# Kernel optimization log

Hardware: AMD Instinct MI355X
Metric: run time of the kernel (lower is better)

## Reference

```python
import jax, jax.numpy as jnp
import numpy as np


def setup_inputs() -> dict:
    key = jax.random.key(0)
    k1, k2, k3 = jax.random.split(key, 3)
    B, S, E = 2, 2048, 2048
    H, O, A = 16, 1024, 128  # heads, codebook options, head_size (E = H*A)
    x = jax.random.normal(k1, (B, S, E), dtype=jnp.float32)
    vq_head_weights = jax.random.normal(k2, (H, O, A), dtype=jnp.float32) * 0.02
    vq_codebooks = jax.random.normal(k3, (H, O, A), dtype=jnp.float32) * 0.02
    temperature = jnp.ones((1,), dtype=jnp.float32)
    return {"x": x, "vq_head_weights": vq_head_weights, "vq_codebooks": vq_codebooks, "temperature": temperature}


def reference(x, vq_head_weights, vq_codebooks, temperature):
    # Training-mode, frozen, use_temperature=True path (straight-through VQ):
    # probs = one_hot(argmax(logits)) + softmax(logits/T) - stop_grad(softmax(logits/T))
    B, S, E = x.shape
    H, O, A = vq_head_weights.shape
    x_prepped = x.reshape(B, S, H, A)
    logits = jnp.einsum('bsha,hoa->bsho', x_prepped, vq_head_weights)
    probs = jax.nn.softmax(logits / temperature[0], axis=-1)
    argmax = jnp.argmax(logits, axis=-1)  # [B,S,H]
    hard_probs = jax.nn.one_hot(argmax, O, dtype=logits.dtype)
    probs = hard_probs + probs - jax.lax.stop_gradient(probs)
    out = jnp.einsum('bsho,hoa->bsha', probs, vq_codebooks)
    return out.reshape(B, S, E)
```

## Files before the change

kernel.cpp:

```cpp
#include <hip/hip_runtime.h>

typedef _Float16 half8 __attribute__((ext_vector_type(8)));
typedef float    f32x16 __attribute__((ext_vector_type(16)));

constexpr int kH = 16;
constexpr int kO = 1024;
constexpr int kA = 128;
constexpr int kBS = 4096;
constexpr int MTILE = 64;
constexpr int NITER = 16;

typedef const __attribute__((address_space(1))) uint32_t* gas_ptr;
typedef __attribute__((address_space(3))) uint32_t* las_ptr;

__global__ void split_w(const float* __restrict__ w, ushort* __restrict__ wp) {
    const int lane = threadIdx.x & 63;
    const int gw   = blockIdx.x * 4 + (threadIdx.x >> 6);
    const int ks   = lane >> 3;
    const int half = (lane >> 2) & 1;
    const int j    = (2 * lane) & 7;
#pragma unroll
    for (int q = 0; q < 4; ++q) {
        int r = gw * 4 + q;
        int h = r >> 10, o = r & 1023, t = o >> 5, o31 = o & 31;
        float2 v = *(const float2*)(w + r * kA + lane * 2);
        _Float16 h0 = (_Float16)v.x, h1 = (_Float16)v.y;
        _Float16 l0 = (_Float16)(v.x - (float)h0), l1 = (_Float16)(v.y - (float)h1);
        ushort2 hv = { __builtin_bit_cast(ushort, h0), __builtin_bit_cast(ushort, h1) };
        ushort2 lv = { __builtin_bit_cast(ushort, l0), __builtin_bit_cast(ushort, l1) };
        ushort* d = wp + (h * 32 + t) * 8192 + ks * 512 + (half * 32 + o31) * 8 + j;
        *(ushort2*)d = hv;
        *(ushort2*)(d + 4096) = lv;
    }
}

__launch_bounds__(256, 2)
__global__ void vq_argmax_gather(const float* __restrict__ x,
                                 const ushort* __restrict__ wp,
                                 const float* __restrict__ cb,
                                 float* __restrict__ out) {
    __shared__ ushort wtile[2][2][8192];
    __shared__ float red_max[2][MTILE];
    __shared__ int   red_idx[2][MTILE];

    const int tid   = threadIdx.x;
    const int lane  = tid & 63;
    const int wv    = tid >> 6;
    const int nhalf = wv >> 1;
    const int mtile = wv & 1;
    const int bid   = blockIdx.x;
    const int h  = ((bid & 7) << 1) | ((bid >> 3) & 1);
    const int p0 = (bid >> 4) * MTILE;

    const int l31  = lane & 31;
    const int half = lane >> 5;

    const ushort* wh_base = wp + h * 32 * 8192;

    auto stage = [&](int it, int buf) {
#pragma unroll
        for (int q = 0; q < 8; ++q) {
            int c   = wv * 8 + q;
            int nh  = c >> 4, rem = c & 15;
            const ushort* g = wh_base + (nh * 16 + it) * 8192 + rem * 512 + lane * 8;
            ushort* l = &wtile[buf][nh][rem * 512];
            __builtin_amdgcn_global_load_lds((gas_ptr)(const void*)g,
                                             (las_ptr)(void*)l, 16, 0, 0);
        }
    };

    stage(0, 0);

    const int mrow = p0 + mtile * 32 + l31;
    const float* xbase = x + (mrow * kH + h) * kA + half * 8;
    half8 xh[8], xl[8];
#pragma unroll
    for (int ks = 0; ks < 8; ++ks) {
        float4 v0 = *(const float4*)(xbase + ks * 16);
        float4 v1 = *(const float4*)(xbase + ks * 16 + 4);
        float va[8] = { v0.x, v0.y, v0.z, v0.w, v1.x, v1.y, v1.z, v1.w };
        half8 hi, lo;
#pragma unroll
        for (int j = 0; j < 8; ++j) {
            _Float16 hj = (_Float16)va[j];
            hi[j] = hj;
            lo[j] = (_Float16)(va[j] - (float)hj);
        }
        xh[ks] = hi; xl[ks] = lo;
    }

    float best = -1e30f;
    int   bidx = 0;
    const int nwb = nhalf * (kO / 2);

    __syncthreads();

    for (int it = 0; it < NITER; ++it) {
        const int cur = it & 1;
        if (it + 1 < NITER) stage(it + 1, cur ^ 1);

        const ushort* lbase = &wtile[cur][nhalf][lane * 8];
        half8 wh[8], wl[8];
#pragma unroll
        for (int ks = 0; ks < 8; ++ks) {
            wh[ks] = *(const half8*)(lbase + ks * 512);
            wl[ks] = *(const half8*)(lbase + 4096 + ks * 512);
        }
        f32x16 acc = {};
#pragma unroll
        for (int ks = 0; ks < 8; ++ks)
            acc = __builtin_amdgcn_mfma_f32_32x32x16_f16(wh[ks], xh[ks], acc, 0, 0, 0);
#pragma unroll
        for (int ks = 0; ks < 8; ++ks)
            acc = __builtin_amdgcn_mfma_f32_32x32x16_f16(wh[ks], xl[ks], acc, 0, 0, 0);
#pragma unroll
        for (int ks = 0; ks < 8; ++ks)
            acc = __builtin_amdgcn_mfma_f32_32x32x16_f16(wl[ks], xh[ks], acc, 0, 0, 0);

        float lv = acc[0];
        int   lr = 0;
#pragma unroll
        for (int r = 1; r < 16; ++r) {
            if (acc[r] > lv) { lv = acc[r]; lr = r; }
        }
        int li = nwb + it * 32 + 4 * half + (lr & 3) + 8 * (lr >> 2);
        if (lv > best) { best = lv; bidx = li; }

        __syncthreads();
    }

    {
        float om = __shfl_xor(best, 32, 64);
        int   oi = __shfl_xor(bidx, 32, 64);
        if (om > best || (om == best && oi < bidx)) { best = om; bidx = oi; }
    }
    if (half == 0) {
        red_max[nhalf][mtile * 32 + l31] = best;
        red_idx[nhalf][mtile * 32 + l31] = bidx;
    }
    __syncthreads();

    for (int i = tid; i < MTILE * 32; i += 256) {
        int row = i >> 5, ch = i & 31;
        float m0 = red_max[0][row], m1 = red_max[1][row];
        int o = (m1 > m0) ? red_idx[1][row] : red_idx[0][row];
        float4 v = *(const float4*)(cb + (h * kO + o) * kA + ch * 4);
        *(float4*)(out + ((p0 + row) * kH + h) * kA + ch * 4) = v;
    }
}

extern "C" void kernel_launch(void* const* d_in, const int* in_sizes, int n_in,
                              void* d_out, int out_size, void* d_ws, size_t ws_size,
                              hipStream_t stream) {
    const float* x  = (const float*)d_in[0];
    const float* w  = (const float*)d_in[1];
    const float* cb = (const float*)d_in[2];
    float* out = (float*)d_out;

    ushort* wpacked = (ushort*)d_ws;

    split_w<<<dim3(1024), dim3(256), 0, stream>>>(w, wpacked);
    vq_argmax_gather<<<dim3((kBS / MTILE) * kH), dim3(256), 0, stream>>>(x, wpacked, cb, out);
}
```

Measured before the change: 155.2 us.

## Enlarge M tile to 256 rows, 8 waves, 4-deep LDS weight pipeline

```diff
diff --git a/kernel.cpp b/kernel.cpp
--- a/kernel.cpp
+++ b/kernel.cpp
@@ -7,8 +7,9 @@
 constexpr int kO = 1024;
 constexpr int kA = 128;
 constexpr int kBS = 4096;
-constexpr int MTILE = 64;
+constexpr int MTILE = 256;
 constexpr int NITER = 16;
+constexpr int NBUF = 4;
 
 typedef const __attribute__((address_space(1))) uint32_t* gas_ptr;
 typedef __attribute__((address_space(3))) uint32_t* las_ptr;
@@ -34,20 +35,26 @@
     }
 }
 
-__launch_bounds__(256, 2)
+#define PHASE_SYNC(N) do {                                        \
+    asm volatile("s_waitcnt vmcnt(" #N ")" ::: "memory");         \
+    __builtin_amdgcn_s_barrier();                                 \
+    asm volatile("" ::: "memory");                                \
+  } while (0)
+
+__launch_bounds__(512, 2)
 __global__ void vq_argmax_gather(const float* __restrict__ x,
                                  const ushort* __restrict__ wp,
                                  const float* __restrict__ cb,
                                  float* __restrict__ out) {
-    __shared__ ushort wtile[2][2][8192];
+    __shared__ ushort wtile[NBUF][2][8192];
     __shared__ float red_max[2][MTILE];
     __shared__ int   red_idx[2][MTILE];
 
     const int tid   = threadIdx.x;
     const int lane  = tid & 63;
     const int wv    = tid >> 6;
-    const int nhalf = wv >> 1;
-    const int mtile = wv & 1;
+    const int nhalf = wv >> 2;
+    const int msub  = wv & 3;
     const int bid   = blockIdx.x;
     const int h  = ((bid & 7) << 1) | ((bid >> 3) & 1);
     const int p0 = (bid >> 4) * MTILE;
@@ -59,8 +66,8 @@
 
     auto stage = [&](int it, int buf) {
 #pragma unroll
-        for (int q = 0; q < 8; ++q) {
-            int c   = wv * 8 + q;
+        for (int q = 0; q < 4; ++q) {
+            int c   = wv * 4 + q;
             int nh  = c >> 4, rem = c & 15;
             const ushort* g = wh_base + (nh * 16 + it) * 8192 + rem * 512 + lane * 8;
             ushort* l = &wtile[buf][nh][rem * 512];
@@ -69,78 +76,100 @@
         }
     };
 
-    stage(0, 0);
+    stage(0, 0); stage(1, 1); stage(2, 2);
+    asm volatile("" ::: "memory");
 
-    const int mrow = p0 + mtile * 32 + l31;
-    const float* xbase = x + (mrow * kH + h) * kA + half * 8;
-    half8 xh[8], xl[8];
-#pragma unroll
-    for (int ks = 0; ks < 8; ++ks) {
-        float4 v0 = *(const float4*)(xbase + ks * 16);
-        float4 v1 = *(const float4*)(xbase + ks * 16 + 4);
+    const int mrow0 = p0 + msub * 64 + l31;
+    const float* xb0 = x + (mrow0 * kH + h) * kA + half * 8;
+    const float* xb1 = xb0 + 32 * kH * kA;
+    half8 xh0[8], xl0[8], xh1[8], xl1[8];
+    auto cvt8 = [&](const float* p, half8& hi, half8& lo) {
+        float4 v0 = *(const float4*)(p);
+        float4 v1 = *(const float4*)(p + 4);
         float va[8] = { v0.x, v0.y, v0.z, v0.w, v1.x, v1.y, v1.z, v1.w };
-        half8 hi, lo;
 #pragma unroll
         for (int j = 0; j < 8; ++j) {
             _Float16 hj = (_Float16)va[j];
             hi[j] = hj;
             lo[j] = (_Float16)(va[j] - (float)hj);
         }
-        xh[ks] = hi; xl[ks] = lo;
+    };
+#pragma unroll
+    for (int ks = 0; ks < 8; ++ks) {
+        cvt8(xb0 + ks * 16, xh0[ks], xl0[ks]);
+        cvt8(xb1 + ks * 16, xh1[ks], xl1[ks]);
     }
 
-    float best = -1e30f;
-    int   bidx = 0;
+    float best0 = -1e30f, best1 = -1e30f;
+    int   bidx0 = 0,      bidx1 = 0;
     const int nwb = nhalf * (kO / 2);
 
-    __syncthreads();
-
-    for (int it = 0; it < NITER; ++it) {
-        const int cur = it & 1;
-        if (it + 1 < NITER) stage(it + 1, cur ^ 1);
-
-        const ushort* lbase = &wtile[cur][nhalf][lane * 8];
-        half8 wh[8], wl[8];
+    auto compute = [&](int it) {
+        const int buf = it & 3;
+        const ushort* lbase = &wtile[buf][nhalf][lane * 8];
+        f32x16 acc0 = {}, acc1 = {};
+        __builtin_amdgcn_s_setprio(1);
 #pragma unroll
         for (int ks = 0; ks < 8; ++ks) {
-            wh[ks] = *(const half8*)(lbase + ks * 512);
-            wl[ks] = *(const half8*)(lbase + 4096 + ks * 512);
+            half8 wh = *(const half8*)(lbase + ks * 512);
+            acc0 = __builtin_amdgcn_mfma_f32_32x32x16_f16(wh, xh0[ks], acc0, 0, 0, 0);
+            acc1 = __builtin_amdgcn_mfma_f32_32x32x16_f16(wh, xh1[ks], acc1, 0, 0, 0);
         }
-        f32x16 acc = {};
 #pragma unroll
-        for (int ks = 0; ks < 8; ++ks)
-            acc = __builtin_amdgcn_mfma_f32_32x32x16_f16(wh[ks], xh[ks], acc, 0, 0, 0);
+        for (int ks = 0; ks < 8; ++ks) {
+            half8 wh = *(const half8*)(lbase + ks * 512);
+            acc0 = __builtin_amdgcn_mfma_f32_32x32x16_f16(wh, xl0[ks], acc0, 0, 0, 0);
+            acc1 = __builtin_amdgcn_mfma_f32_32x32x16_f16(wh, xl1[ks], acc1, 0, 0, 0);
+        }
 #pragma unroll
-        for (int ks = 0; ks < 8; ++ks)
-            acc = __builtin_amdgcn_mfma_f32_32x32x16_f16(wh[ks], xl[ks], acc, 0, 0, 0);
+        for (int ks = 0; ks < 8; ++ks) {
+            half8 wl = *(const half8*)(lbase + 4096 + ks * 512);
+            acc0 = __builtin_amdgcn_mfma_f32_32x32x16_f16(wl, xh0[ks], acc0, 0, 0, 0);
+            acc1 = __builtin_amdgcn_mfma_f32_32x32x16_f16(wl, xh1[ks], acc1, 0, 0, 0);
+        }
+        __builtin_amdgcn_s_setprio(0);
+
+        float lv0 = acc0[0]; int lr0 = 0;
 #pragma unroll
-        for (int ks = 0; ks < 8; ++ks)
-            acc = __builtin_amdgcn_mfma_f32_32x32x16_f16(wl[ks], xh[ks], acc, 0, 0, 0);
+        for (int r = 1; r < 16; ++r)
+            if (acc0[r] > lv0) { lv0 = acc0[r]; lr0 = r; }
+        int li0 = nwb + it * 32 + 4 * half + (lr0 & 3) + 8 * (lr0 >> 2);
+        if (lv0 > best0) { best0 = lv0; bidx0 = li0; }
 
-        float lv = acc[0];
-        int   lr = 0;
+        float lv1 = acc1[0]; int lr1 = 0;
 #pragma unroll
-        for (int r = 1; r < 16; ++r) {
-            if (acc[r] > lv) { lv = acc[r]; lr = r; }
-        }
-        int li = nwb + it * 32 + 4 * half + (lr & 3) + 8 * (lr >> 2);
-        if (lv > best) { best = lv; bidx = li; }
+        for (int r = 1; r < 16; ++r)
+            if (acc1[r] > lv1) { lv1 = acc1[r]; lr1 = r; }
+        int li1 = nwb + it * 32 + 4 * half + (lr1 & 3) + 8 * (lr1 >> 2);
+        if (lv1 > best1) { best1 = lv1; bidx1 = li1; }
+    };
 
-        __syncthreads();
+    for (int it = 0; it < NITER - 3; ++it) {
+        PHASE_SYNC(8);
+        stage(it + 3, (it + 3) & 3);
+        compute(it);
     }
+    PHASE_SYNC(8); compute(NITER - 3);
+    PHASE_SYNC(4); compute(NITER - 2);
+    PHASE_SYNC(0); compute(NITER - 1);
 
     {
-        float om = __shfl_xor(best, 32, 64);
-        int   oi = __shfl_xor(bidx, 32, 64);
-        if (om > best || (om == best && oi < bidx)) { best = om; bidx = oi; }
+        float om = __shfl_xor(best0, 32, 64);
+        int   oi = __shfl_xor(bidx0, 32, 64);
+        if (om > best0 || (om == best0 && oi < bidx0)) { best0 = om; bidx0 = oi; }
+        om = __shfl_xor(best1, 32, 64);
+        oi = __shfl_xor(bidx1, 32, 64);
+        if (om > best1 || (om == best1 && oi < bidx1)) { best1 = om; bidx1 = oi; }
     }
     if (half == 0) {
-        red_max[nhalf][mtile * 32 + l31] = best;
-        red_idx[nhalf][mtile * 32 + l31] = bidx;
+        red_max[nhalf][msub * 64 + l31]      = best0;
+        red_idx[nhalf][msub * 64 + l31]      = bidx0;
+        red_max[nhalf][msub * 64 + 32 + l31] = best1;
+        red_idx[nhalf][msub * 64 + 32 + l31] = bidx1;
     }
     __syncthreads();
 
-    for (int i = tid; i < MTILE * 32; i += 256) {
+    for (int i = tid; i < MTILE * 32; i += 512) {
         int row = i >> 5, ch = i & 31;
         float m0 = red_max[0][row], m1 = red_max[1][row];
         int o = (m1 > m0) ? red_idx[1][row] : red_idx[0][row];
@@ -160,5 +189,5 @@
     ushort* wpacked = (ushort*)d_ws;
 
     split_w<<<dim3(1024), dim3(256), 0, stream>>>(w, wpacked);
-    vq_argmax_gather<<<dim3((kBS / MTILE) * kH), dim3(256), 0, stream>>>(x, wpacked, cb, out);
+    vq_argmax_gather<<<dim3((kBS / MTILE) * kH), dim3(512), 0, stream>>>(x, wpacked, cb, out);
 }
```

Measured after the change: 148.9 us. 4.1% less time.

## Load weight fragments directly from global into registers, drop LDS staging

Applied to the files above, without the earlier changes.

```diff
diff --git a/kernel.cpp b/kernel.cpp
--- a/kernel.cpp
+++ b/kernel.cpp
@@ -9,9 +9,6 @@
 constexpr int kBS = 4096;
 constexpr int MTILE = 64;
 constexpr int NITER = 16;
-
-typedef const __attribute__((address_space(1))) uint32_t* gas_ptr;
-typedef __attribute__((address_space(3))) uint32_t* las_ptr;
 
 __global__ void split_w(const float* __restrict__ w, ushort* __restrict__ wp) {
     const int lane = threadIdx.x & 63;
@@ -34,12 +31,12 @@
     }
 }
 
-__launch_bounds__(256, 2)
+__launch_bounds__(256, 4)
 __global__ void vq_argmax_gather(const float* __restrict__ x,
                                  const ushort* __restrict__ wp,
                                  const float* __restrict__ cb,
                                  float* __restrict__ out) {
-    __shared__ ushort wtile[2][2][8192];
+    __shared__ ushort xl_lds[4][8][512];
     __shared__ float red_max[2][MTILE];
     __shared__ int   red_idx[2][MTILE];
 
@@ -47,7 +44,7 @@
     const int lane  = tid & 63;
     const int wv    = tid >> 6;
     const int nhalf = wv >> 1;
-    const int mtile = wv & 1;
+    const int msub  = wv & 1;
     const int bid   = blockIdx.x;
     const int h  = ((bid & 7) << 1) | ((bid >> 3) & 1);
     const int p0 = (bid >> 4) * MTILE;
@@ -55,29 +52,20 @@
     const int l31  = lane & 31;
     const int half = lane >> 5;
 
-    const ushort* wh_base = wp + h * 32 * 8192;
+    const ushort* wb = wp + (h * 32 + nhalf * 16) * 8192 + lane * 8;
 
-    auto stage = [&](int it, int buf) {
+    half8 A[8];
 #pragma unroll
-        for (int q = 0; q < 8; ++q) {
-            int c   = wv * 8 + q;
-            int nh  = c >> 4, rem = c & 15;
-            const ushort* g = wh_base + (nh * 16 + it) * 8192 + rem * 512 + lane * 8;
-            ushort* l = &wtile[buf][nh][rem * 512];
-            __builtin_amdgcn_global_load_lds((gas_ptr)(const void*)g,
-                                             (las_ptr)(void*)l, 16, 0, 0);
-        }
-    };
+    for (int ks = 0; ks < 8; ++ks)
+        A[ks] = *(const half8*)(wb + ks * 512);
 
-    stage(0, 0);
-
-    const int mrow = p0 + mtile * 32 + l31;
-    const float* xbase = x + (mrow * kH + h) * kA + half * 8;
-    half8 xh[8], xl[8];
+    const int mrow = p0 + msub * 32 + l31;
+    const float* xb = x + (mrow * kH + h) * kA + half * 8;
+    half8 xh[8];
 #pragma unroll
     for (int ks = 0; ks < 8; ++ks) {
-        float4 v0 = *(const float4*)(xbase + ks * 16);
-        float4 v1 = *(const float4*)(xbase + ks * 16 + 4);
+        float4 v0 = *(const float4*)(xb + ks * 16);
+        float4 v1 = *(const float4*)(xb + ks * 16 + 4);
         float va[8] = { v0.x, v0.y, v0.z, v0.w, v1.x, v1.y, v1.z, v1.w };
         half8 hi, lo;
 #pragma unroll
@@ -86,47 +74,46 @@
             hi[j] = hj;
             lo[j] = (_Float16)(va[j] - (float)hj);
         }
-        xh[ks] = hi; xl[ks] = lo;
+        xh[ks] = hi;
+        *(half8*)&xl_lds[wv][ks][lane * 8] = lo;
     }
 
     float best = -1e30f;
     int   bidx = 0;
     const int nwb = nhalf * (kO / 2);
 
-    __syncthreads();
-
     for (int it = 0; it < NITER; ++it) {
-        const int cur = it & 1;
-        if (it + 1 < NITER) stage(it + 1, cur ^ 1);
-
-        const ushort* lbase = &wtile[cur][nhalf][lane * 8];
-        half8 wh[8], wl[8];
-#pragma unroll
-        for (int ks = 0; ks < 8; ++ks) {
-            wh[ks] = *(const half8*)(lbase + ks * 512);
-            wl[ks] = *(const half8*)(lbase + 4096 + ks * 512);
-        }
+        const ushort* tb = wb + it * 8192;
         f32x16 acc = {};
 #pragma unroll
         for (int ks = 0; ks < 8; ++ks)
-            acc = __builtin_amdgcn_mfma_f32_32x32x16_f16(wh[ks], xh[ks], acc, 0, 0, 0);
+            acc = __builtin_amdgcn_mfma_f32_32x32x16_f16(A[ks], xh[ks], acc, 0, 0, 0);
+#pragma unroll
+        for (int ks = 0; ks < 8; ++ks) {
+            half8 xlk = *(const half8*)&xl_lds[wv][ks][lane * 8];
+            acc = __builtin_amdgcn_mfma_f32_32x32x16_f16(A[ks], xlk, acc, 0, 0, 0);
+        }
+        half8 Bf[8];
 #pragma unroll
         for (int ks = 0; ks < 8; ++ks)
-            acc = __builtin_amdgcn_mfma_f32_32x32x16_f16(wh[ks], xl[ks], acc, 0, 0, 0);
+            Bf[ks] = *(const half8*)(tb + 4096 + ks * 512);
 #pragma unroll
         for (int ks = 0; ks < 8; ++ks)
-            acc = __builtin_amdgcn_mfma_f32_32x32x16_f16(wl[ks], xh[ks], acc, 0, 0, 0);
+            acc = __builtin_amdgcn_mfma_f32_32x32x16_f16(Bf[ks], xh[ks], acc, 0, 0, 0);
+        if (it + 1 < NITER) {
+            const ushort* nb = wb + (it + 1) * 8192;
+#pragma unroll
+            for (int ks = 0; ks < 8; ++ks)
+                A[ks] = *(const half8*)(nb + ks * 512);
+        }
 
         float lv = acc[0];
         int   lr = 0;
 #pragma unroll
-        for (int r = 1; r < 16; ++r) {
+        for (int r = 1; r < 16; ++r)
             if (acc[r] > lv) { lv = acc[r]; lr = r; }
-        }
         int li = nwb + it * 32 + 4 * half + (lr & 3) + 8 * (lr >> 2);
         if (lv > best) { best = lv; bidx = li; }
-
-        __syncthreads();
     }
 
     {
@@ -135,8 +122,8 @@
         if (om > best || (om == best && oi < bidx)) { best = om; bidx = oi; }
     }
     if (half == 0) {
-        red_max[nhalf][mtile * 32 + l31] = best;
-        red_idx[nhalf][mtile * 32 + l31] = bidx;
+        red_max[nhalf][msub * 32 + l31] = best;
+        red_idx[nhalf][msub * 32 + l31] = bidx;
     }
     __syncthreads();
 
```

After: 153.5 us. Within noise of the previous version (-1.1%).
